# Kernel tuning notes

Measured on AMD Instinct MI355X. Metric: run time of the kernel, lower is better.

## Reference

```python
import jax, jax.numpy as jnp
import numpy as np

B, S, H, D = 8, 1024, 32, 128
SM_SCALE = D ** -0.5


def _make_bias(dtype=jnp.float32):
    # causal mask [1, 1, S, S]
    causal = jnp.tril(jnp.ones((S, S), dtype=bool))[None, None, :, :]
    attn_mask = jnp.ones((B, S), dtype=bool).at[:, S // 2:].set(False)
    pad = attn_mask[:, None, None, :]  # [B,1,1,S]
    combined = jnp.logical_and(causal, pad)  # [B,1,S,S]
    neg = jnp.finfo(dtype).min
    return jnp.where(combined, jnp.asarray(0.0, dtype), jnp.asarray(neg, dtype))


def setup_inputs() -> dict:
    key = jax.random.key(0)
    kq, kk, kv = jax.random.split(key, 3)
    query = jax.random.normal(kq, (B, S, H, D), dtype=jnp.float32)
    k = jax.random.normal(kk, (B, S, H, D), dtype=jnp.float32)
    v = jax.random.normal(kv, (B, S, H, D), dtype=jnp.float32)
    bias = _make_bias()
    return {"query": query, "key": k, "value": v, "bias": bias}


def reference(query, key, value, bias):
    # query/key/value: [B, S, H, D]; bias: [B, 1, Sq, Sk] (broadcast over heads)
    scores = jnp.einsum("bqhd,bkhd->bhqk", query, key) * SM_SCALE + bias
    attn = jax.nn.softmax(scores, axis=-1)
    out = jnp.einsum("bhqk,bkhd->bqhd", attn, value)
    return out
```

## Files before the change

kernel.cpp:

```cpp
#include <hip/hip_runtime.h>
#include <stdint.h>

typedef __attribute__((ext_vector_type(8))) short short8;
typedef __attribute__((ext_vector_type(8))) unsigned short us8;
typedef __attribute__((ext_vector_type(4))) float f32x4;
typedef __attribute__((ext_vector_type(4))) unsigned short usvec4;

#define B_ 8
#define S_ 1024
#define H_ 32
#define D_ 128
#define NSTEP (S_ / 32)

static __device__ __forceinline__ unsigned short f2bf(float f) {
  uint32_t u = __builtin_bit_cast(uint32_t, f);
  u += 0x7FFFu + ((u >> 16) & 1u);
  return (unsigned short)(u >> 16);
}

__global__ __launch_bounds__(256)
void kv_pre(const float* __restrict__ Kp, const float* __restrict__ Vp,
            unsigned short* __restrict__ Kw, unsigned short* __restrict__ Vw)
{
  const int flat   = blockIdx.x * 256 + threadIdx.x;
  const int tid2   = flat & 511;
  const int bhstep = flat >> 9;
  const int step   = bhstep & (NSTEP - 1);
  const int bhi    = bhstep >> 5;
  const int h      = bhi & (H_ - 1);
  const int b      = bhi >> 5;

  const size_t strideS = (size_t)H_ * D_;
  const size_t base    = ((size_t)b * S_) * strideS + (size_t)h * D_;
  const size_t dst     = (size_t)bhstep * 4096 + (size_t)tid2 * 8;

  {
    const int f = tid2 >> 7, tile = (tid2 >> 6) & 1, ln = tid2 & 63;
    const int cc = ln & 15, qd = ln >> 4;
    const float* src = Kp + base + (size_t)(step * 32 + tile * 16 + cc) * strideS + f * 32 + qd * 8;
    float4 a = *(const float4*)src;
    float4 c4 = *(const float4*)(src + 4);
    us8 r;
    r[0] = f2bf(a.x);  r[1] = f2bf(a.y);  r[2] = f2bf(a.z);  r[3] = f2bf(a.w);
    r[4] = f2bf(c4.x); r[5] = f2bf(c4.y); r[6] = f2bf(c4.z); r[7] = f2bf(c4.w);
    *(us8*)(Kw + dst) = r;
  }
  {
    const int t = tid2 >> 6, ln = tid2 & 63;
    const int cv = ln & 15, qv = ln >> 4;
    const float* src = Vp + base + (size_t)(step * 32 + qv * 8) * strideS + t * 16 + cv;
    us8 r;
#pragma unroll
    for (int j = 0; j < 8; ++j) r[j] = f2bf(src[(size_t)j * strideS]);
    *(us8*)(Vw + dst) = r;
  }
}

__global__ __launch_bounds__(256)
void mask_pre(const float* __restrict__ BiasP, uint32_t* __restrict__ Mw)
{
  const int idx = blockIdx.x * 256 + threadIdx.x;
  const float NEGT = -1e37f;
  const float* src = BiasP + (size_t)idx * 32;
  uint32_t mbits = 0;
#pragma unroll
  for (int j = 0; j < 8; ++j) {
    float4 v = *(const float4*)(src + j * 4);
    mbits |= (uint32_t)(v.x > NEGT) << (j * 4 + 0);
    mbits |= (uint32_t)(v.y > NEGT) << (j * 4 + 1);
    mbits |= (uint32_t)(v.z > NEGT) << (j * 4 + 2);
    mbits |= (uint32_t)(v.w > NEGT) << (j * 4 + 3);
  }
  Mw[idx] = mbits;
}

__global__ __launch_bounds__(256, 2)
void fa_fwd2(const float* __restrict__ Qp,
             const unsigned short* __restrict__ Kw,
             const unsigned short* __restrict__ Vw,
             const uint32_t* __restrict__ Mw,
             float* __restrict__ Op)
{
  __shared__ __align__(16) unsigned short klds[2][4096];
  __shared__ __align__(16) unsigned short vlds[2][4096];
  __shared__ uint32_t vmask_sh;

  const int tid  = threadIdx.x;
  const int lane = tid & 63;
  const int w    = tid >> 6;
  const int quad = lane >> 4;
  const int c    = lane & 15;

  const int qt = blockIdx.x;
  const int h  = blockIdx.y;
  const int b  = blockIdx.z;
  const int qi = qt * 64 + w * 16 + c;

  const size_t strideS = (size_t)H_ * D_;
  const size_t bh  = ((size_t)b * S_) * strideS + (size_t)h * D_;
  const size_t kvb = (size_t)(b * H_ + h) * ((size_t)NSTEP * 4096);

  short8 qf[4];
  {
    const float* qrow = Qp + bh + (size_t)qi * strideS;
#pragma unroll
    for (int f = 0; f < 4; ++f) {
      float4 a  = *(const float4*)(qrow + f * 32 + quad * 8);
      float4 bv = *(const float4*)(qrow + f * 32 + quad * 8 + 4);
      short8 r;
      r[0] = (short)f2bf(a.x);  r[1] = (short)f2bf(a.y);
      r[2] = (short)f2bf(a.z);  r[3] = (short)f2bf(a.w);
      r[4] = (short)f2bf(bv.x); r[5] = (short)f2bf(bv.y);
      r[6] = (short)f2bf(bv.z); r[7] = (short)f2bf(bv.w);
      qf[f] = r;
    }
  }

  const uint32_t* mrow = Mw + ((size_t)b * S_ + qi) * NSTEP;

  uint32_t myv = 0;
#pragma unroll
  for (int i = 0; i < 8; ++i) {
    uint4 v = *(const uint4*)(mrow + i * 4);
    myv |= (uint32_t)(v.x != 0) << (i * 4 + 0);
    myv |= (uint32_t)(v.y != 0) << (i * 4 + 1);
    myv |= (uint32_t)(v.z != 0) << (i * 4 + 2);
    myv |= (uint32_t)(v.w != 0) << (i * 4 + 3);
  }
  if (tid == 0) vmask_sh = 0;
  __syncthreads();
  {
    uint32_t wor = myv;
#pragma unroll
    for (int d = 1; d < 64; d <<= 1) wor |= __shfl_xor(wor, d);
    if (lane == 0) atomicOr(&vmask_sh, wor);
  }
  __syncthreads();
  const uint32_t bmask = vmask_sh;

  float m  = -INFINITY;
  float ll = 0.f;
  f32x4 acc[8];
#pragma unroll
  for (int t = 0; t < 8; ++t) acc[t] = (f32x4){0.f, 0.f, 0.f, 0.f};

  const float SL2E = 0.08838834764831845f * 1.4426950408889634f;

  auto stage = [&](int bufi, int stp) {
    const unsigned short* kg = Kw + kvb + (size_t)stp * 4096 + w * 1024 + lane * 8;
    const unsigned short* vg = Vw + kvb + (size_t)stp * 4096 + w * 1024 + lane * 8;
    unsigned short* kl = &klds[bufi][w * 1024];
    unsigned short* vl = &vlds[bufi][w * 1024];
    __builtin_amdgcn_global_load_lds(
        (const __attribute__((address_space(1))) void*)kg,
        (__attribute__((address_space(3))) void*)kl, 16, 0, 0);
    __builtin_amdgcn_global_load_lds(
        (const __attribute__((address_space(1))) void*)(kg + 512),
        (__attribute__((address_space(3))) void*)(kl + 512), 16, 0, 0);
    __builtin_amdgcn_global_load_lds(
        (const __attribute__((address_space(1))) void*)vg,
        (__attribute__((address_space(3))) void*)vl, 16, 0, 0);
    __builtin_amdgcn_global_load_lds(
        (const __attribute__((address_space(1))) void*)(vg + 512),
        (__attribute__((address_space(3))) void*)(vl + 512), 16, 0, 0);
  };

  int st  = bmask ? (__ffs(bmask) - 1) : -1;
  int cur = 0;
  uint32_t rem = bmask;
  uint32_t mw_ = 0;

  if (st >= 0) {
    mw_ = mrow[st];
    stage(0, st);
    asm volatile("s_waitcnt vmcnt(0)" ::: "memory");
    __builtin_amdgcn_s_barrier();
    asm volatile("" ::: "memory");
  }

  while (st >= 0) {
    rem &= rem - 1;
    const int nst = rem ? (__ffs(rem) - 1) : -1;

    uint32_t mnxt = 0;
    if (nst >= 0) {
      mnxt = mrow[nst];
      stage(cur ^ 1, nst);
    }

    const int m0 = (int)((mw_ >> (quad * 4)) & 15u);
    const int m1 = (int)((mw_ >> (16 + quad * 4)) & 15u);
    const int wvv = __any(m0 | m1);

    if (wvv) {
      const unsigned short* kb_ = klds[cur];
      const unsigned short* vb_ = vlds[cur];

      f32x4 st0 = (f32x4){0.f, 0.f, 0.f, 0.f};
      f32x4 st1 = (f32x4){0.f, 0.f, 0.f, 0.f};
      __builtin_amdgcn_s_setprio(1);
#pragma unroll
      for (int f = 0; f < 4; ++f) {
        short8 ka  = *(const short8*)(kb_ + f * 1024 + lane * 8);
        short8 kbt = *(const short8*)(kb_ + f * 1024 + 512 + lane * 8);
        st0 = __builtin_amdgcn_mfma_f32_16x16x32_bf16(ka,  qf[f], st0, 0, 0, 0);
        st1 = __builtin_amdgcn_mfma_f32_16x16x32_bf16(kbt, qf[f], st1, 0, 0, 0);
      }
      __builtin_amdgcn_s_setprio(0);

      float x0[4], x1[4];
      float mt = -INFINITY;
#pragma unroll
      for (int r = 0; r < 4; ++r) {
        x0[r] = ((m0 >> r) & 1) ? st0[r] * SL2E : -INFINITY;
        x1[r] = ((m1 >> r) & 1) ? st1[r] * SL2E : -INFINITY;
        mt = fmaxf(mt, fmaxf(x0[r], x1[r]));
      }
      mt = fmaxf(mt, __shfl_xor(mt, 16));
      mt = fmaxf(mt, __shfl_xor(mt, 32));

      if (!__all(mt <= m + 8.f)) {
        const float mn    = fmaxf(m, mt);
        const float alpha = exp2f(m - mn);
        m = mn;
        ll *= alpha;
#pragma unroll
        for (int t = 0; t < 8; ++t) {
          acc[t][0] *= alpha; acc[t][1] *= alpha;
          acc[t][2] *= alpha; acc[t][3] *= alpha;
        }
      }

      float p0[4], p1[4];
      float lt = 0.f;
#pragma unroll
      for (int r = 0; r < 4; ++r) {
        p0[r] = exp2f(x0[r] - m);
        p1[r] = exp2f(x1[r] - m);
        lt += p0[r] + p1[r];
      }
      lt += __shfl_xor(lt, 16);
      lt += __shfl_xor(lt, 32);
      ll += lt;

      int i0, i1, i2, i3;
      asm("v_cvt_pk_bf16_f32 %0, %1, %2" : "=v"(i0) : "v"(p0[0]), "v"(p0[1]));
      asm("v_cvt_pk_bf16_f32 %0, %1, %2" : "=v"(i1) : "v"(p0[2]), "v"(p0[3]));
      asm("v_cvt_pk_bf16_f32 %0, %1, %2" : "=v"(i2) : "v"(p1[0]), "v"(p1[1]));
      asm("v_cvt_pk_bf16_f32 %0, %1, %2" : "=v"(i3) : "v"(p1[2]), "v"(p1[3]));

      const int srcA = ((quad & 1) << 5) + c;
      const int srcB = srcA + 16;
      const int hiT  = quad >> 1;

      int sA, sB, w0, w1, w2, w3;
      sA = __shfl(i0, srcA); sB = __shfl(i2, srcA); w0 = hiT ? sB : sA;
      sA = __shfl(i1, srcA); sB = __shfl(i3, srcA); w1 = hiT ? sB : sA;
      sA = __shfl(i0, srcB); sB = __shfl(i2, srcB); w2 = hiT ? sB : sA;
      sA = __shfl(i1, srcB); sB = __shfl(i3, srcB); w3 = hiT ? sB : sA;

      union { int u[4]; short8 v; } pf;
      pf.u[0] = w0; pf.u[1] = w1; pf.u[2] = w2; pf.u[3] = w3;

      __builtin_amdgcn_s_setprio(1);
#pragma unroll
      for (int t = 0; t < 8; ++t) {
        short8 vf = *(const short8*)(vb_ + t * 512 + lane * 8);
        acc[t] = __builtin_amdgcn_mfma_f32_16x16x32_bf16(vf, pf.v, acc[t], 0, 0, 0);
      }
      __builtin_amdgcn_s_setprio(0);
    }

    if (nst >= 0) {
      asm volatile("s_waitcnt vmcnt(0)" ::: "memory");
      __builtin_amdgcn_s_barrier();
      asm volatile("" ::: "memory");
    }
    cur ^= 1;
    st = nst;
    mw_ = mnxt;
  }

  const float rl = 1.0f / ll;
  float* orow = Op + bh + (size_t)qi * strideS;
#pragma unroll
  for (int t = 0; t < 8; ++t) {
    float4 o;
    o.x = acc[t][0] * rl; o.y = acc[t][1] * rl;
    o.z = acc[t][2] * rl; o.w = acc[t][3] * rl;
    *(float4*)(orow + t * 16 + quad * 4) = o;
  }
}

__global__ __launch_bounds__(256, 2)
void fa_fwd(const float* __restrict__ Qp,
            const float* __restrict__ Kp,
            const float* __restrict__ Vp,
            const float* __restrict__ BiasP,
            float* __restrict__ Op)
{
  __shared__ __align__(16) unsigned short klds[32 * 136];
  __shared__ __align__(16) unsigned short vlds[8 * 520];

  const int tid  = threadIdx.x;
  const int lane = tid & 63;
  const int w    = tid >> 6;
  const int quad = lane >> 4;
  const int c    = lane & 15;

  const int qt = blockIdx.x;
  const int h  = blockIdx.y;
  const int b  = blockIdx.z;
  const int qi = qt * 64 + w * 16 + c;

  const size_t strideS = (size_t)H_ * D_;
  const size_t bh = ((size_t)b * S_) * strideS + (size_t)h * D_;

  short8 qf[4];
  {
    const float* qrow = Qp + bh + (size_t)qi * strideS;
#pragma unroll
    for (int f = 0; f < 4; ++f) {
      float4 a  = *(const float4*)(qrow + f * 32 + quad * 8);
      float4 bv = *(const float4*)(qrow + f * 32 + quad * 8 + 4);
      short8 r;
      r[0] = (short)f2bf(a.x);  r[1] = (short)f2bf(a.y);
      r[2] = (short)f2bf(a.z);  r[3] = (short)f2bf(a.w);
      r[4] = (short)f2bf(bv.x); r[5] = (short)f2bf(bv.y);
      r[6] = (short)f2bf(bv.z); r[7] = (short)f2bf(bv.w);
      qf[f] = r;
    }
  }

  const float* brow = BiasP + ((size_t)b * S_ + qi) * S_;
  const float NEGT = -1e37f;

  float m  = -INFINITY;
  float ll = 0.f;
  f32x4 acc[8];
#pragma unroll
  for (int t = 0; t < 8; ++t) acc[t] = (f32x4){0.f, 0.f, 0.f, 0.f};

  const float SL2E = 0.08838834764831845f * 1.4426950408889634f;
  const float L2E  = 1.4426950408889634f;

  for (int ks = 0; ks < S_; ks += 32) {
    float4 b0f = *(const float4*)(brow + ks + quad * 4);
    float4 b1f = *(const float4*)(brow + ks + 16 + quad * 4);
    float b0a[4] = {b0f.x, b0f.y, b0f.z, b0f.w};
    float b1a[4] = {b1f.x, b1f.y, b1f.z, b1f.w};
    int lv = 0;
#pragma unroll
    for (int r = 0; r < 4; ++r) lv |= (b0a[r] > NEGT) | (b1a[r] > NEGT);
    const int wv = __any(lv);
    const int bvalid = __syncthreads_or(wv);
    if (!bvalid) continue;

    {
      const int kk = tid >> 3;
      const int dc = tid & 7;

      const float* krow = Kp + bh + (size_t)(ks + kk) * strideS + dc * 16;
      unsigned short kb16[16];
#pragma unroll
      for (int i = 0; i < 4; ++i) {
        float4 kv = *(const float4*)(krow + i * 4);
        kb16[i*4+0] = f2bf(kv.x); kb16[i*4+1] = f2bf(kv.y);
        kb16[i*4+2] = f2bf(kv.z); kb16[i*4+3] = f2bf(kv.w);
      }
      usvec4* kdst = (usvec4*)(klds + kk * 136 + dc * 16);
#pragma unroll
      for (int i = 0; i < 4; ++i)
        kdst[i] = (usvec4){kb16[i*4+0], kb16[i*4+1], kb16[i*4+2], kb16[i*4+3]};

      const float* vrow = Vp + bh + (size_t)(ks + kk) * strideS + dc * 16;
      const int base = dc * 520 + (kk >> 3) * 128 + (kk & 7);
#pragma unroll
      for (int i = 0; i < 4; ++i) {
        float4 vv = *(const float4*)(vrow + i * 4);
        vlds[base + (i*4+0)*8] = f2bf(vv.x);
        vlds[base + (i*4+1)*8] = f2bf(vv.y);
        vlds[base + (i*4+2)*8] = f2bf(vv.z);
        vlds[base + (i*4+3)*8] = f2bf(vv.w);
      }
    }
    __syncthreads();

    if (wv) {
      f32x4 st0 = (f32x4){0.f, 0.f, 0.f, 0.f};
      f32x4 st1 = (f32x4){0.f, 0.f, 0.f, 0.f};
#pragma unroll
      for (int f = 0; f < 4; ++f) {
        short8 ka = *(const short8*)(klds + c * 136 + f * 32 + quad * 8);
        short8 kb = *(const short8*)(klds + (16 + c) * 136 + f * 32 + quad * 8);
        st0 = __builtin_amdgcn_mfma_f32_16x16x32_bf16(ka, qf[f], st0, 0, 0, 0);
        st1 = __builtin_amdgcn_mfma_f32_16x16x32_bf16(kb, qf[f], st1, 0, 0, 0);
      }

      float x0[4], x1[4];
      float mt = -INFINITY;
#pragma unroll
      for (int r = 0; r < 4; ++r) {
        x0[r] = (b0a[r] > NEGT) ? fmaf(b0a[r], L2E, st0[r] * SL2E) : -INFINITY;
        x1[r] = (b1a[r] > NEGT) ? fmaf(b1a[r], L2E, st1[r] * SL2E) : -INFINITY;
        mt = fmaxf(mt, fmaxf(x0[r], x1[r]));
      }
      mt = fmaxf(mt, __shfl_xor(mt, 16));
      mt = fmaxf(mt, __shfl_xor(mt, 32));
      const float mn    = fmaxf(m, mt);
      const float alpha = exp2f(m - mn);
      m = mn;

      float p0[4], p1[4];
      float lt = 0.f;
#pragma unroll
      for (int r = 0; r < 4; ++r) {
        p0[r] = exp2f(x0[r] - mn);
        p1[r] = exp2f(x1[r] - mn);
        lt += p0[r] + p1[r];
      }
      lt += __shfl_xor(lt, 16);
      lt += __shfl_xor(lt, 32);
      ll = ll * alpha + lt;

#pragma unroll
      for (int t = 0; t < 8; ++t) {
        acc[t][0] *= alpha; acc[t][1] *= alpha;
        acc[t][2] *= alpha; acc[t][3] *= alpha;
      }

      const int i0 = (int)(((uint32_t)f2bf(p0[0])) | ((uint32_t)f2bf(p0[1]) << 16));
      const int i1 = (int)(((uint32_t)f2bf(p0[2])) | ((uint32_t)f2bf(p0[3]) << 16));
      const int i2 = (int)(((uint32_t)f2bf(p1[0])) | ((uint32_t)f2bf(p1[1]) << 16));
      const int i3 = (int)(((uint32_t)f2bf(p1[2])) | ((uint32_t)f2bf(p1[3]) << 16));

      const int srcA = ((quad & 1) << 5) + c;
      const int srcB = srcA + 16;
      const int hiT  = quad >> 1;

      int sA, sB, w0, w1, w2, w3;
      sA = __shfl(i0, srcA); sB = __shfl(i2, srcA); w0 = hiT ? sB : sA;
      sA = __shfl(i1, srcA); sB = __shfl(i3, srcA); w1 = hiT ? sB : sA;
      sA = __shfl(i0, srcB); sB = __shfl(i2, srcB); w2 = hiT ? sB : sA;
      sA = __shfl(i1, srcB); sB = __shfl(i3, srcB); w3 = hiT ? sB : sA;

      union { int u[4]; short8 v; } pf;
      pf.u[0] = w0; pf.u[1] = w1; pf.u[2] = w2; pf.u[3] = w3;

#pragma unroll
      for (int t = 0; t < 8; ++t) {
        short8 vf = *(const short8*)(vlds + t * 520 + lane * 8);
        acc[t] = __builtin_amdgcn_mfma_f32_16x16x32_bf16(vf, pf.v, acc[t], 0, 0, 0);
      }
    }
    __syncthreads();
  }

  const float rl = 1.0f / ll;
  float* orow = Op + bh + (size_t)qi * strideS;
#pragma unroll
  for (int t = 0; t < 8; ++t) {
    float4 o;
    o.x = acc[t][0] * rl; o.y = acc[t][1] * rl;
    o.z = acc[t][2] * rl; o.w = acc[t][3] * rl;
    *(float4*)(orow + t * 16 + quad * 4) = o;
  }
}

extern "C" void kernel_launch(void* const* d_in, const int* in_sizes, int n_in,
                              void* d_out, int out_size, void* d_ws, size_t ws_size,
                              hipStream_t stream) {
  const float* q    = (const float*)d_in[0];
  const float* k    = (const float*)d_in[1];
  const float* v    = (const float*)d_in[2];
  const float* bias = (const float*)d_in[3];
  float* out = (float*)d_out;

  const size_t KW_BYTES = (size_t)B_ * H_ * NSTEP * 4096 * 2;
  const size_t MW_BYTES = (size_t)B_ * S_ * NSTEP * 4;
  const size_t NEED     = 2 * KW_BYTES + MW_BYTES;

  dim3 grid(S_ / 64, H_, B_);
  if (ws_size >= NEED) {
    unsigned short* Kw = (unsigned short*)d_ws;
    unsigned short* Vw = (unsigned short*)((char*)d_ws + KW_BYTES);
    uint32_t*       Mw = (uint32_t*)((char*)d_ws + 2 * KW_BYTES);
    kv_pre<<<(B_ * H_ * NSTEP * 512) / 256, 256, 0, stream>>>(k, v, Kw, Vw);
    mask_pre<<<(B_ * S_ * NSTEP) / 256, 256, 0, stream>>>(bias, Mw);
    fa_fwd2<<<grid, 256, 0, stream>>>(q, Kw, Vw, Mw, out);
  } else {
    fa_fwd<<<grid, 256, 0, stream>>>(q, k, v, bias, out);
  }
}
```

Baseline: 551.2 us.

## Skip K/V conversion for fully masked key blocks and defer row-sum reduction

The mask preprocessing kernel now also records, per batch and 32-key step, whether any query row uses that key block. It runs before the K/V conversion kernel, which skips fully masked steps and so avoids reading and converting K/V for padded keys. The attention kernel's launch bound is raised to 4 blocks per CU to ask for higher occupancy, and the cross-lane row-sum shuffles move out of the inner loop to a single reduction at the end. This adds a memset, atomics and a kernel dependency, and relies on the attention kernel never reading the skipped workspace blocks; the tighter register budget could cause spills.

```diff
diff --git a/kernel.cpp b/kernel.cpp
--- a/kernel.cpp
+++ b/kernel.cpp
@@ -19,8 +19,40 @@
 }
 
 __global__ __launch_bounds__(256)
+void mask_pre(const float* __restrict__ BiasP, uint32_t* __restrict__ Mw,
+              uint32_t* __restrict__ Su)
+{
+  __shared__ uint32_t su_sh[32];
+  const int tid = threadIdx.x;
+  if (tid < 32) su_sh[tid] = 0;
+  __syncthreads();
+
+  const int idx = blockIdx.x * 256 + tid;
+  const float NEGT = -1e37f;
+  const float* src = BiasP + (size_t)idx * 32;
+  uint32_t mbits = 0;
+#pragma unroll
+  for (int j = 0; j < 8; ++j) {
+    float4 v = *(const float4*)(src + j * 4);
+    mbits |= (uint32_t)(v.x > NEGT) << (j * 4 + 0);
+    mbits |= (uint32_t)(v.y > NEGT) << (j * 4 + 1);
+    mbits |= (uint32_t)(v.z > NEGT) << (j * 4 + 2);
+    mbits |= (uint32_t)(v.w > NEGT) << (j * 4 + 3);
+  }
+  Mw[idx] = mbits;
+
+  uint32_t used = (mbits != 0) ? 1u : 0u;
+  used |= __shfl_xor(used, 32);
+  if ((tid & 63) < 32 && used) atomicOr(&su_sh[tid & 31], 1u);
+  __syncthreads();
+  const int b32 = (blockIdx.x >> 7) * 32;
+  if (tid < 32 && su_sh[tid]) atomicOr(&Su[b32 + tid], 1u);
+}
+
+__global__ __launch_bounds__(256)
 void kv_pre(const float* __restrict__ Kp, const float* __restrict__ Vp,
-            unsigned short* __restrict__ Kw, unsigned short* __restrict__ Vw)
+            unsigned short* __restrict__ Kw, unsigned short* __restrict__ Vw,
+            const uint32_t* __restrict__ Su)
 {
   const int flat   = blockIdx.x * 256 + threadIdx.x;
   const int tid2   = flat & 511;
@@ -29,6 +61,8 @@
   const int bhi    = bhstep >> 5;
   const int h      = bhi & (H_ - 1);
   const int b      = bhi >> 5;
+
+  if (!Su[b * 32 + step]) return;
 
   const size_t strideS = (size_t)H_ * D_;
   const size_t base    = ((size_t)b * S_) * strideS + (size_t)h * D_;
@@ -56,25 +90,7 @@
   }
 }
 
-__global__ __launch_bounds__(256)
-void mask_pre(const float* __restrict__ BiasP, uint32_t* __restrict__ Mw)
-{
-  const int idx = blockIdx.x * 256 + threadIdx.x;
-  const float NEGT = -1e37f;
-  const float* src = BiasP + (size_t)idx * 32;
-  uint32_t mbits = 0;
-#pragma unroll
-  for (int j = 0; j < 8; ++j) {
-    float4 v = *(const float4*)(src + j * 4);
-    mbits |= (uint32_t)(v.x > NEGT) << (j * 4 + 0);
-    mbits |= (uint32_t)(v.y > NEGT) << (j * 4 + 1);
-    mbits |= (uint32_t)(v.z > NEGT) << (j * 4 + 2);
-    mbits |= (uint32_t)(v.w > NEGT) << (j * 4 + 3);
-  }
-  Mw[idx] = mbits;
-}
-
-__global__ __launch_bounds__(256, 2)
+__global__ __launch_bounds__(256, 4)
 void fa_fwd2(const float* __restrict__ Qp,
              const unsigned short* __restrict__ Kw,
              const unsigned short* __restrict__ Vw,
@@ -239,8 +255,6 @@
         p1[r] = exp2f(x1[r] - m);
         lt += p0[r] + p1[r];
       }
-      lt += __shfl_xor(lt, 16);
-      lt += __shfl_xor(lt, 32);
       ll += lt;
 
       int i0, i1, i2, i3;
@@ -281,6 +295,8 @@
     mw_ = mnxt;
   }
 
+  ll += __shfl_xor(ll, 16);
+  ll += __shfl_xor(ll, 32);
   const float rl = 1.0f / ll;
   float* orow = Op + bh + (size_t)qi * strideS;
 #pragma unroll
@@ -478,15 +494,18 @@
 
   const size_t KW_BYTES = (size_t)B_ * H_ * NSTEP * 4096 * 2;
   const size_t MW_BYTES = (size_t)B_ * S_ * NSTEP * 4;
-  const size_t NEED     = 2 * KW_BYTES + MW_BYTES;
+  const size_t SU_BYTES = (size_t)B_ * NSTEP * 4;
+  const size_t NEED     = 2 * KW_BYTES + MW_BYTES + SU_BYTES;
 
   dim3 grid(S_ / 64, H_, B_);
   if (ws_size >= NEED) {
     unsigned short* Kw = (unsigned short*)d_ws;
     unsigned short* Vw = (unsigned short*)((char*)d_ws + KW_BYTES);
     uint32_t*       Mw = (uint32_t*)((char*)d_ws + 2 * KW_BYTES);
-    kv_pre<<<(B_ * H_ * NSTEP * 512) / 256, 256, 0, stream>>>(k, v, Kw, Vw);
-    mask_pre<<<(B_ * S_ * NSTEP) / 256, 256, 0, stream>>>(bias, Mw);
+    uint32_t*       Su = (uint32_t*)((char*)d_ws + 2 * KW_BYTES + MW_BYTES);
+    hipMemsetAsync(Su, 0, SU_BYTES, stream);
+    mask_pre<<<(B_ * S_ * NSTEP) / 256, 256, 0, stream>>>(bias, Mw, Su);
+    kv_pre<<<(B_ * H_ * NSTEP * 512) / 256, 256, 0, stream>>>(k, v, Kw, Vw, Su);
     fa_fwd2<<<grid, 256, 0, stream>>>(q, Kw, Vw, Mw, out);
   } else {
     fa_fwd<<<grid, 256, 0, stream>>>(q, k, v, bias, out);
```

Measured after the change: 515.6 us. 1.07x faster.
